# Performance work log

Hardware: AMD Instinct MI355X
Metric: run time of the kernel (lower is better)

Reference implementation:

```python
import jax, jax.numpy as jnp
import numpy as np

N_NODES = 50000
EMBED_DIM = 128
HIDDEN_DIM = 64
N_EDGES = 1600000
TEMP = 1.0


def setup_inputs() -> dict:
    key = jax.random.key(0)
    k1, k2, k3, k4 = jax.random.split(key, 4)
    node_embed = jax.random.normal(k1, (N_NODES, EMBED_DIM), dtype=jnp.float32)
    edge_index = jax.random.randint(k2, (2, N_EDGES), 0, N_NODES, dtype=jnp.int64)
    # MLP params (Linear(2*D, H) -> ReLU -> Linear(H, 1)); PyTorch-style fan-in scaling
    W1 = jax.random.normal(k3, (2 * EMBED_DIM, HIDDEN_DIM), dtype=jnp.float32) * (1.0 / np.sqrt(2 * EMBED_DIM))
    b1 = jnp.zeros((HIDDEN_DIM,), dtype=jnp.float32)
    W2 = jax.random.normal(k4, (HIDDEN_DIM, 1), dtype=jnp.float32) * (1.0 / np.sqrt(HIDDEN_DIM))
    b2 = jnp.zeros((1,), dtype=jnp.float32)
    return {"node_embed": node_embed, "edge_index": edge_index,
            "W1": W1, "b1": b1, "W2": W2, "b2": b2}


def reference(node_embed, edge_index, W1, b1, W2, b2):
    row, col = edge_index[0], edge_index[1]
    # gather + concat: [E, 2*D]
    edge_feat = jnp.concatenate([node_embed[row], node_embed[col]], axis=1)
    # tiny 2-layer MLP (dropout = identity in eval mode)
    h = jax.nn.relu(edge_feat @ W1 + b1)            # [E, H]
    edge_logits = (h @ W2 + b2)[:, 0]               # [E]
    # gumbel-sigmoid: difference of two Gumbel(0,1) samples (= logistic noise)
    nk = jax.random.key(42)
    nk1, nk2 = jax.random.split(nk)
    noise = jax.random.gumbel(nk1, edge_logits.shape, dtype=edge_logits.dtype) \
          - jax.random.gumbel(nk2, edge_logits.shape, dtype=edge_logits.dtype)
    edge_probs = jax.nn.sigmoid((edge_logits + noise) / TEMP)
    return edge_probs
```

## Files before the change

### kernel.cpp

```cpp
#include <hip/hip_runtime.h>
#include <hip/hip_bf16.h>
#include <stdint.h>

#define N_NODES 50000
#define NE      1600000
#define DIM     128
#define HID     64

typedef __attribute__((ext_vector_type(8))) short bf16x8;
typedef __attribute__((ext_vector_type(4))) float f32x4;

struct TF2 { uint32_t a, b; };

__host__ __device__ constexpr uint32_t rotl32(uint32_t x, int d) {
  return (x << d) | (x >> (32 - d));
}

__host__ __device__ constexpr TF2 threefry(uint32_t k0, uint32_t k1,
                                           uint32_t c0, uint32_t c1) {
  uint32_t ks[3] = { k0, k1, k0 ^ k1 ^ 0x1BD11BDAu };
  uint32_t x0 = c0 + ks[0], x1 = c1 + ks[1];
  const int rot[2][4] = { {13, 15, 26, 6}, {17, 29, 16, 24} };
  for (int i = 0; i < 5; ++i) {
    for (int r = 0; r < 4; ++r) {
      x0 += x1;
      x1 = rotl32(x1, rot[i & 1][r]);
      x1 ^= x0;
    }
    x0 += ks[(i + 1) % 3];
    x1 += ks[(i + 2) % 3] + (uint32_t)(i + 1);
  }
  return { x0, x1 };
}

constexpr TF2 SPA = threefry(0u, 42u, 0u, 0u);
constexpr TF2 SPB = threefry(0u, 42u, 0u, 1u);
constexpr uint32_t NK1_0 = SPA.a, NK1_1 = SPA.b;
constexpr uint32_t NK2_0 = SPB.a, NK2_1 = SPB.b;

__device__ inline float gumbel_elem(uint32_t k0, uint32_t k1, uint32_t i) {
  TF2 t = threefry(k0, k1, 0u, i);
  uint32_t bits = t.a ^ t.b;
  float f = __uint_as_float((bits >> 9) | 0x3f800000u) - 1.0f;
  float u = fmaxf(1.1754943508222875e-38f, f + 1.1754943508222875e-38f);
  return -__logf(-__logf(u));
}

__device__ inline unsigned short f2bf_rne(float f) {
  uint32_t u = __float_as_uint(f);
  uint32_t r = (u + 0x7fffu + ((u >> 16) & 1u)) >> 16;
  return (unsigned short)r;
}

#define NPB_M  64
#define NBLKN  ((N_NODES + NPB_M - 1) / NPB_M)
#define WT_LD  136

__global__ __launch_bounds__(256, 4)
void node_mfma_kernel(const float* __restrict__ node,
                      const float* __restrict__ W1,
                      const float* __restrict__ b1,
                      unsigned short* __restrict__ A_tab,
                      unsigned short* __restrict__ B_tab) {
  __shared__ unsigned short wt[128 * WT_LD];

  const int tid  = threadIdx.x;
  const int lane = tid & 63;
  const int w    = tid >> 6;
  const int c    = lane & 15;
  const int b    = lane >> 4;
  const int v0   = blockIdx.x * NPB_M;

  for (int idx = tid; idx < 128 * 128; idx += 256) {
    const int k  = idx >> 7;
    const int np = idx & 127;
    const float wv = W1[((size_t)((np >> 6) * 128 + k)) * HID + (np & 63)];
    wt[np * WT_LD + k] = f2bf_rne(wv);
  }
  __syncthreads();

  const int vld = min(v0 + w * 16 + c, N_NODES - 1);
  const float4* __restrict__ xrp = (const float4*)(node + (size_t)vld * DIM);
  float4 xx[8];
#pragma unroll
  for (int kk = 0; kk < 4; ++kk) {
    xx[2 * kk]     = xrp[kk * 8 + b * 2];
    xx[2 * kk + 1] = xrp[kk * 8 + b * 2 + 1];
  }

  f32x4 acc[8];
#pragma unroll
  for (int nt = 0; nt < 8; ++nt) acc[nt] = (f32x4){0.f, 0.f, 0.f, 0.f};

#pragma unroll
  for (int kk = 0; kk < 4; ++kk) {
    const float4 x0 = xx[2 * kk];
    const float4 x1 = xx[2 * kk + 1];
    const float xs[8] = { x0.x, x0.y, x0.z, x0.w, x1.x, x1.y, x1.z, x1.w };
    bf16x8 af;
#pragma unroll
    for (int j = 0; j < 8; ++j) af[j] = (short)f2bf_rne(xs[j]);

#pragma unroll
    for (int nt = 0; nt < 8; ++nt) {
      const bf16x8 bf =
          *(const bf16x8*)&wt[(nt * 16 + c) * WT_LD + kk * 32 + b * 8];
      acc[nt] = __builtin_amdgcn_mfma_f32_16x16x32_bf16(af, bf, acc[nt], 0, 0, 0);
    }
  }

#pragma unroll
  for (int nt = 0; nt < 8; ++nt) {
    const int np = nt * 16 + c;
    const float badd = (np < HID) ? b1[np] : 0.0f;
    unsigned short* __restrict__ base =
        (np < HID) ? (A_tab + np) : (B_tab + (np - HID));
#pragma unroll
    for (int r = 0; r < 4; ++r) {
      const int v = v0 + w * 16 + b * 4 + r;
      if (v < N_NODES) base[(size_t)v * HID] = f2bf_rne(acc[nt][r] + badd);
    }
  }
}

#define EPB    256
#define NBATCH (NE / EPB)

__global__ __launch_bounds__(256, 2)
void edge_kernel_dma(const int* __restrict__ ei,
                     const unsigned short* __restrict__ A_tab,
                     const unsigned short* __restrict__ B_tab,
                     const float* __restrict__ W2,
                     const float* __restrict__ b2,
                     float* __restrict__ out) {
  __shared__ uint4 buf[4096];

  const int lane = threadIdx.x & 63;
  const int w    = threadIdx.x >> 6;
  const int l7   = lane & 7;
  const float bias2 = b2[0];

  uint4* wbuf = buf + w * 1024;

  for (int bt = blockIdx.x; bt < NBATCH; bt += gridDim.x) {
    const int e0 = bt * EPB + w * 64;

#pragma unroll
    for (int j = 0; j < 16; ++j) {
      const int sgl = j * 64 + lane;
      const int ed  = sgl >> 4;
      const int s   = sgl & 15;
      const int q   = (s & 8) | ((s & 7) ^ (ed & 7));
      const int idx = __builtin_nontemporal_load(ei + e0 + ed + (q < 8 ? 0 : NE));
      const unsigned short* g =
          (q < 8 ? A_tab : B_tab) + (size_t)idx * HID + (q & 7) * 8;
      __builtin_amdgcn_global_load_lds(
          (const __attribute__((address_space(1))) uint32_t*)g,
          (__attribute__((address_space(3))) uint32_t*)(wbuf + j * 64),
          16, 0, 0);
    }

    const int e = e0 + lane;
    const float g1 = gumbel_elem(NK1_0, NK1_1, (uint32_t)e);
    const float g2 = gumbel_elem(NK2_0, NK2_1, (uint32_t)e);

    asm volatile("s_waitcnt vmcnt(0)" ::: "memory");
    __builtin_amdgcn_sched_barrier(0);

    float logit = bias2;
    const int tbase = lane * 16;
#pragma unroll
    for (int qq = 0; qq < 8; ++qq) {
      const int slo = qq ^ l7;
      const uint4 a4 = wbuf[tbase + slo];
      const uint4 b4 = wbuf[tbase + 8 + slo];
      const uint32_t* au = (const uint32_t*)&a4;
      const uint32_t* bu = (const uint32_t*)&b4;
#pragma unroll
      for (int t = 0; t < 4; ++t) {
        const float a0 = __uint_as_float(au[t] << 16);
        const float a1 = __uint_as_float(au[t] & 0xffff0000u);
        const float b0 = __uint_as_float(bu[t] << 16);
        const float b1v = __uint_as_float(bu[t] & 0xffff0000u);
        const int jj = qq * 8 + t * 2;
        logit = fmaf(fmaxf(a0 + b0, 0.0f),  W2[jj],     logit);
        logit = fmaf(fmaxf(a1 + b1v, 0.0f), W2[jj + 1], logit);
      }
    }

    const float z = logit + g1 - g2;
    __builtin_nontemporal_store(1.0f / (1.0f + __expf(-z)), out + e);
  }
}

__global__ __launch_bounds__(256, 4)
void edge_prune_fallback(const float* __restrict__ node,
                         const int*   __restrict__ ei,
                         const float* __restrict__ W1,
                         const float* __restrict__ b1,
                         const float* __restrict__ W2,
                         const float* __restrict__ b2,
                         float*       __restrict__ out) {
  const int tid    = blockIdx.x * blockDim.x + threadIdx.x;
  const int stride = gridDim.x * blockDim.x;
  const float bias2 = b2[0];

  for (int e = tid; e < NE; e += stride) {
    const int r = ei[e];
    const int c = ei[NE + e];
    const float4* __restrict__ up = (const float4*)(node + (size_t)r * DIM);
    const float4* __restrict__ vp = (const float4*)(node + (size_t)c * DIM);

    float h[HID];
#pragma unroll
    for (int j = 0; j < HID; ++j) h[j] = b1[j];

#pragma unroll 1
    for (int dd = 0; dd < DIM / 4; ++dd) {
      const float4 xu = up[dd];
      const float4 xv = vp[dd];
      const float xs[8] = { xu.x, xu.y, xu.z, xu.w, xv.x, xv.y, xv.z, xv.w };
#pragma unroll
      for (int k = 0; k < 8; ++k) {
        const int drow = (k < 4) ? (dd * 4 + k) : (DIM + dd * 4 + (k - 4));
        const float4* __restrict__ wrow = (const float4*)(W1 + drow * HID);
        const float x = xs[k];
#pragma unroll
        for (int j4 = 0; j4 < HID / 4; ++j4) {
          const float4 w = wrow[j4];
          h[j4 * 4 + 0] = fmaf(x, w.x, h[j4 * 4 + 0]);
          h[j4 * 4 + 1] = fmaf(x, w.y, h[j4 * 4 + 1]);
          h[j4 * 4 + 2] = fmaf(x, w.z, h[j4 * 4 + 2]);
          h[j4 * 4 + 3] = fmaf(x, w.w, h[j4 * 4 + 3]);
        }
      }
    }

    float logit = bias2;
#pragma unroll
    for (int j = 0; j < HID; ++j) logit = fmaf(fmaxf(h[j], 0.0f), W2[j], logit);

    const float g1 = gumbel_elem(NK1_0, NK1_1, (uint32_t)e);
    const float g2 = gumbel_elem(NK2_0, NK2_1, (uint32_t)e);
    const float z  = logit + g1 - g2;
    out[e] = 1.0f / (1.0f + __expf(-z));
  }
}

extern "C" void kernel_launch(void* const* d_in, const int* in_sizes, int n_in,
                              void* d_out, int out_size, void* d_ws, size_t ws_size,
                              hipStream_t stream) {
  const float* node = (const float*)d_in[0];
  const int*   ei   = (const int*)  d_in[1];
  const float* W1   = (const float*)d_in[2];
  const float* b1   = (const float*)d_in[3];
  const float* W2   = (const float*)d_in[4];
  const float* b2   = (const float*)d_in[5];
  float* out = (float*)d_out;

  const size_t tab_bytes = (size_t)N_NODES * HID * sizeof(unsigned short);
  if (ws_size >= 2 * tab_bytes) {
    unsigned short* A_tab = (unsigned short*)d_ws;
    unsigned short* B_tab = A_tab + (size_t)N_NODES * HID;
    node_mfma_kernel<<<dim3(NBLKN), dim3(256), 0, stream>>>(
        node, W1, b1, A_tab, B_tab);
    edge_kernel_dma<<<dim3(512), dim3(256), 0, stream>>>(
        ei, A_tab, B_tab, W2, b2, out);
  } else {
    edge_prune_fallback<<<dim3(1024), dim3(256), 0, stream>>>(
        node, ei, W1, b1, W2, b2, out);
  }
}
```

Before: 67.94 us.

## Switch edge kernel to per-wave dynamic work stealing via atomic counter

```diff
diff --git a/kernel.cpp b/kernel.cpp
--- a/kernel.cpp
+++ b/kernel.cpp
@@ -61,7 +61,10 @@
                       const float* __restrict__ W1,
                       const float* __restrict__ b1,
                       unsigned short* __restrict__ A_tab,
-                      unsigned short* __restrict__ B_tab) {
+                      unsigned short* __restrict__ B_tab,
+                      uint32_t* cnt) {
+  if (cnt && blockIdx.x == 0 && threadIdx.x == 0) *cnt = 0u;
+
   __shared__ unsigned short wt[128 * WT_LD];
 
   const int tid  = threadIdx.x;
@@ -123,8 +126,7 @@
   }
 }
 
-#define EPB    256
-#define NBATCH (NE / EPB)
+#define NUNIT (NE / 256)
 
 __global__ __launch_bounds__(256, 2)
 void edge_kernel_dma(const int* __restrict__ ei,
@@ -132,7 +134,8 @@
                      const unsigned short* __restrict__ B_tab,
                      const float* __restrict__ W2,
                      const float* __restrict__ b2,
-                     float* __restrict__ out) {
+                     float* __restrict__ out,
+                     uint32_t* cnt) {
   __shared__ uint4 buf[4096];
 
   const int lane = threadIdx.x & 63;
@@ -142,54 +145,72 @@
 
   uint4* wbuf = buf + w * 1024;
 
-  for (int bt = blockIdx.x; bt < NBATCH; bt += gridDim.x) {
-    const int e0 = bt * EPB + w * 64;
-
-#pragma unroll
-    for (int j = 0; j < 16; ++j) {
-      const int sgl = j * 64 + lane;
-      const int ed  = sgl >> 4;
-      const int s   = sgl & 15;
-      const int q   = (s & 8) | ((s & 7) ^ (ed & 7));
-      const int idx = __builtin_nontemporal_load(ei + e0 + ed + (q < 8 ? 0 : NE));
-      const unsigned short* g =
-          (q < 8 ? A_tab : B_tab) + (size_t)idx * HID + (q & 7) * 8;
-      __builtin_amdgcn_global_load_lds(
-          (const __attribute__((address_space(1))) uint32_t*)g,
-          (__attribute__((address_space(3))) uint32_t*)(wbuf + j * 64),
-          16, 0, 0);
-    }
-
-    const int e = e0 + lane;
-    const float g1 = gumbel_elem(NK1_0, NK1_1, (uint32_t)e);
-    const float g2 = gumbel_elem(NK2_0, NK2_1, (uint32_t)e);
-
-    asm volatile("s_waitcnt vmcnt(0)" ::: "memory");
-    __builtin_amdgcn_sched_barrier(0);
-
-    float logit = bias2;
-    const int tbase = lane * 16;
-#pragma unroll
-    for (int qq = 0; qq < 8; ++qq) {
-      const int slo = qq ^ l7;
-      const uint4 a4 = wbuf[tbase + slo];
-      const uint4 b4 = wbuf[tbase + 8 + slo];
-      const uint32_t* au = (const uint32_t*)&a4;
-      const uint32_t* bu = (const uint32_t*)&b4;
-#pragma unroll
-      for (int t = 0; t < 4; ++t) {
-        const float a0 = __uint_as_float(au[t] << 16);
-        const float a1 = __uint_as_float(au[t] & 0xffff0000u);
-        const float b0 = __uint_as_float(bu[t] << 16);
-        const float b1v = __uint_as_float(bu[t] & 0xffff0000u);
-        const int jj = qq * 8 + t * 2;
-        logit = fmaf(fmaxf(a0 + b0, 0.0f),  W2[jj],     logit);
-        logit = fmaf(fmaxf(a1 + b1v, 0.0f), W2[jj + 1], logit);
+  const int gwave  = blockIdx.x * 4 + w;
+  const int nwaves = gridDim.x * 4;
+  int ustat = gwave;
+
+  for (;;) {
+    int unit;
+    if (cnt) {
+      int t;
+      if (lane == 0) t = (int)atomicAdd(cnt, 1u);
+      unit = __shfl(t, 0);
+    } else {
+      unit = ustat;
+      ustat += nwaves;
+    }
+    if (unit >= NUNIT) break;
+
+#pragma unroll 1
+    for (int it = 0; it < 4; ++it) {
+      const int e0 = unit * 256 + it * 64;
+
+#pragma unroll
+      for (int j = 0; j < 16; ++j) {
+        const int sgl = j * 64 + lane;
+        const int ed  = sgl >> 4;
+        const int s   = sgl & 15;
+        const int q   = (s & 8) | ((s & 7) ^ (ed & 7));
+        const int idx = __builtin_nontemporal_load(ei + e0 + ed + (q < 8 ? 0 : NE));
+        const unsigned short* g =
+            (q < 8 ? A_tab : B_tab) + (size_t)idx * HID + (q & 7) * 8;
+        __builtin_amdgcn_global_load_lds(
+            (const __attribute__((address_space(1))) uint32_t*)g,
+            (__attribute__((address_space(3))) uint32_t*)(wbuf + j * 64),
+            16, 0, 0);
       }
-    }
-
-    const float z = logit + g1 - g2;
-    __builtin_nontemporal_store(1.0f / (1.0f + __expf(-z)), out + e);
+
+      const int e = e0 + lane;
+      const float g1 = gumbel_elem(NK1_0, NK1_1, (uint32_t)e);
+      const float g2 = gumbel_elem(NK2_0, NK2_1, (uint32_t)e);
+
+      asm volatile("s_waitcnt vmcnt(0)" ::: "memory");
+      __builtin_amdgcn_sched_barrier(0);
+
+      float logit = bias2;
+      const int tbase = lane * 16;
+#pragma unroll
+      for (int qq = 0; qq < 8; ++qq) {
+        const int slo = qq ^ l7;
+        const uint4 a4 = wbuf[tbase + slo];
+        const uint4 b4 = wbuf[tbase + 8 + slo];
+        const uint32_t* au = (const uint32_t*)&a4;
+        const uint32_t* bu = (const uint32_t*)&b4;
+#pragma unroll
+        for (int t = 0; t < 4; ++t) {
+          const float a0 = __uint_as_float(au[t] << 16);
+          const float a1 = __uint_as_float(au[t] & 0xffff0000u);
+          const float b0 = __uint_as_float(bu[t] << 16);
+          const float b1v = __uint_as_float(bu[t] & 0xffff0000u);
+          const int jj = qq * 8 + t * 2;
+          logit = fmaf(fmaxf(a0 + b0, 0.0f),  W2[jj],     logit);
+          logit = fmaf(fmaxf(a1 + b1v, 0.0f), W2[jj + 1], logit);
+        }
+      }
+
+      const float z = logit + g1 - g2;
+      __builtin_nontemporal_store(1.0f / (1.0f + __expf(-z)), out + e);
+    }
   }
 }
 
@@ -262,10 +283,13 @@
   if (ws_size >= 2 * tab_bytes) {
     unsigned short* A_tab = (unsigned short*)d_ws;
     unsigned short* B_tab = A_tab + (size_t)N_NODES * HID;
+    uint32_t* cnt = (ws_size >= 2 * tab_bytes + 64)
+                        ? (uint32_t*)((char*)d_ws + 2 * tab_bytes)
+                        : nullptr;
     node_mfma_kernel<<<dim3(NBLKN), dim3(256), 0, stream>>>(
-        node, W1, b1, A_tab, B_tab);
+        node, W1, b1, A_tab, B_tab, cnt);
     edge_kernel_dma<<<dim3(512), dim3(256), 0, stream>>>(
-        ei, A_tab, B_tab, W2, b2, out);
+        ei, A_tab, B_tab, W2, b2, out, cnt);
   } else {
     edge_prune_fallback<<<dim3(1024), dim3(256), 0, stream>>>(
         node, ei, W1, b1, W2, b2, out);
```

Result: slower. 134.1 us (+97.3%).
